# Optimization experiments

Measured on AMD Instinct MI355X. Metric: run time of the kernel, lower is better.

Reference implementation:

```python
import jax, jax.numpy as jnp
import numpy as np

EPS = 1e-5

def _layer_norm(x, w, b):
    mu = jnp.mean(x, axis=-1, keepdims=True)
    var = jnp.mean(jnp.square(x - mu), axis=-1, keepdims=True)
    return (x - mu) * jax.lax.rsqrt(var + EPS) * w + b

def setup_inputs() -> dict:
    B, N, C, H, CH = 1, 256, 128, 4, 32
    key = jax.random.key(0)
    ks = jax.random.split(key, 8)
    s = 0.02
    return {
        "z": jax.random.normal(ks[0], (B, N, N, C), dtype=jnp.float32),
        "pair_mask": jnp.ones((B, N, N), dtype=jnp.float32),
        "ln_w": jnp.ones((C,), dtype=jnp.float32),
        "ln_b": jnp.zeros((C,), dtype=jnp.float32),
        "Wq": jax.random.normal(ks[1], (H * CH, C), dtype=jnp.float32) * s,
        "Wk": jax.random.normal(ks[2], (H * CH, C), dtype=jnp.float32) * s,
        "Wv": jax.random.normal(ks[3], (H * CH, C), dtype=jnp.float32) * s,
        "Wb": jax.random.normal(ks[4], (H, C), dtype=jnp.float32) * s,
        "Wg": jax.random.normal(ks[5], (H * CH, C), dtype=jnp.float32) * s,
        "bg": jnp.zeros((H * CH,), dtype=jnp.float32),
        "Wo": jax.random.normal(ks[6], (C, H * CH), dtype=jnp.float32) * s,
        "bo": jnp.zeros((C,), dtype=jnp.float32),
    }

def reference(z, pair_mask, ln_w, ln_b, Wq, Wk, Wv, Wb, Wg, bg, Wo, bo):
    B, I, J, C = z.shape
    H = Wb.shape[0]
    CH = Wq.shape[0] // H
    zn = _layer_norm(z, ln_w, ln_b)                      # (B,I,J,C)
    q = (zn @ Wq.T).reshape(B, I, J, H, CH)
    k = (zn @ Wk.T).reshape(B, I, J, H, CH)
    v = (zn @ Wv.T).reshape(B, I, J, H, CH)
    bias = zn @ Wb.T                                     # (B,I,J,H) -> per-head pair bias
    g = jax.nn.sigmoid(zn @ Wg.T + bg)                   # (B,I,J,H*CH)
    scale = 1.0 / jnp.sqrt(jnp.asarray(CH, z.dtype))
    # logits[b,h,i,j,k] = q_ij . k_ik / sqrt(CH) + bias[b,h,j,k]
    logits = jnp.einsum('bijhd,bikhd->bhijk', q, k) * scale
    logits = logits + jnp.transpose(bias, (0, 3, 1, 2))[:, :, None, :, :]
    # pair mask: (B,i,j,k) outer product, True = attend
    mask2d = (pair_mask[..., :, None] * pair_mask[..., None, :]) > 0.5
    logits = jnp.where(mask2d[:, None], logits, jnp.asarray(-1e9, logits.dtype))
    probs = jax.nn.softmax(logits, axis=-1)
    o = jnp.einsum('bhijk,bikhd->bijhd', probs, v).reshape(B, I, J, H * CH)
    o = g * o
    return o @ Wo.T + bo
```

## Files before the change

### kernel.cpp

```cpp
#include <hip/hip_runtime.h>
#include <hip/hip_bf16.h>

#define ATT_SCALE 0.17677669529663687f
#define LOG2E     1.4426950408889634f

typedef __attribute__((ext_vector_type(8))) short short8v;
typedef __attribute__((ext_vector_type(4))) float f32x4;
typedef __attribute__((ext_vector_type(16))) float f32x16;

__device__ __forceinline__ short f2bf(float f) {
    unsigned u = __builtin_bit_cast(unsigned, f);
    u = u + 0x7fffu + ((u >> 16) & 1u);
    return (short)(u >> 16);
}
__device__ __forceinline__ float bf2f(short s) {
    unsigned u = ((unsigned)(unsigned short)s) << 16;
    return __builtin_bit_cast(float, u);
}
__device__ __forceinline__ unsigned pk2(float lo, float hi) {
    return (unsigned)(unsigned short)f2bf(lo) |
           ((unsigned)(unsigned short)f2bf(hi) << 16);
}
__device__ __forceinline__ float lo16f(unsigned w) {
    return __builtin_bit_cast(float, w << 16);
}
__device__ __forceinline__ float hi16f(unsigned w) {
    return __builtin_bit_cast(float, w & 0xffff0000u);
}
__device__ __forceinline__ float exp2i(float x) {
    float r;
    asm("v_exp_f32 %0, %1" : "=v"(r) : "v"(x));
    return r;
}
__device__ __forceinline__ unsigned short f2h(float f) {
    _Float16 h = (_Float16)f;
    return __builtin_bit_cast(unsigned short, h);
}
__device__ __forceinline__ float h2f(unsigned short u) {
    return (float)__builtin_bit_cast(_Float16, u);
}

__global__ __launch_bounds__(256) void k_wprep(
    const float* __restrict__ Wq, const float* __restrict__ Wk,
    const float* __restrict__ Wv, const float* __restrict__ Wg,
    const float* __restrict__ Wb, const float* __restrict__ Wo,
    unsigned short* __restrict__ wbf, unsigned short* __restrict__ wbbf,
    unsigned short* __restrict__ wohi, unsigned short* __restrict__ wolo)
{
    int idx = blockIdx.x * 256 + threadIdx.x;
    if (idx < 65536) {
        int m = idx >> 14, e = idx & 16383;
        float v;
        if (m == 0)      v = Wq[e] * (ATT_SCALE * LOG2E);
        else if (m == 1) v = Wk[e];
        else if (m == 2) v = Wv[e];
        else             v = Wg[e];
        wbf[idx] = (unsigned short)f2bf(v);
    } else if (idx < 66048) {
        int e = idx - 65536;
        wbbf[e] = (unsigned short)f2bf(Wb[e]);
    } else if (idx < 82432) {
        int e = idx - 66048;
        float w = Wo[e];
        short hv = f2bf(w);
        wohi[e] = (unsigned short)hv;
        wolo[e] = (unsigned short)f2bf(w - bf2f(hv));
    }
}

__global__ __launch_bounds__(512, 4) void k_lnproj(
    const float* __restrict__ z, const float* __restrict__ lnw,
    const float* __restrict__ lnb,
    const unsigned short* __restrict__ wbf, const unsigned short* __restrict__ wbbf,
    const float* __restrict__ bg,
    unsigned short* __restrict__ q_o, unsigned short* __restrict__ k_o,
    unsigned short* __restrict__ vt_o, unsigned short* __restrict__ g_o,
    unsigned short* __restrict__ bbf)
{
    __shared__ __align__(16) short zn[128][136];
    __shared__ __align__(16) short wstg[8][32][40];

    const int tid  = threadIdx.x;
    const int lane = tid & 63;
    const int wave = tid >> 6;
    const int l15  = lane & 15;
    const int g    = lane >> 4;
    const int wr   = wave >> 2;
    const int wc   = wave & 3;
    const long p0  = (long)blockIdx.x * 128;
    const int xq   = (int)(p0 >> 8);
    const int y0   = (int)(p0 & 255);

    {
        const int r = tid >> 2, q4 = tid & 3;
        const float* zrow = z + (p0 + r) * 128 + q4 * 32;
        float4 xv[8];
        float s1 = 0.f, s2 = 0.f;
#pragma unroll
        for (int m = 0; m < 8; ++m) {
            xv[m] = *(const float4*)(zrow + m * 4);
            s1 += xv[m].x + xv[m].y + xv[m].z + xv[m].w;
            s2 += xv[m].x * xv[m].x + xv[m].y * xv[m].y +
                  xv[m].z * xv[m].z + xv[m].w * xv[m].w;
        }
        s1 += __shfl_xor(s1, 1); s2 += __shfl_xor(s2, 1);
        s1 += __shfl_xor(s1, 2); s2 += __shfl_xor(s2, 2);
        float mu  = s1 * 0.0078125f;
        float inv = rsqrtf(s2 * 0.0078125f - mu * mu + 1e-5f);
#pragma unroll
        for (int mm = 0; mm < 4; ++mm) {
            float4 a = xv[2 * mm], b = xv[2 * mm + 1];
            const float* wp = lnw + q4 * 32 + mm * 8;
            const float* bp = lnb + q4 * 32 + mm * 8;
            float4 w0 = *(const float4*)wp, w1 = *(const float4*)(wp + 4);
            float4 b0 = *(const float4*)bp, b1 = *(const float4*)(bp + 4);
            uint4 uu;
            uu.x = pk2((a.x - mu) * inv * w0.x + b0.x, (a.y - mu) * inv * w0.y + b0.y);
            uu.y = pk2((a.z - mu) * inv * w0.z + b0.z, (a.w - mu) * inv * w0.w + b0.w);
            uu.z = pk2((b.x - mu) * inv * w1.x + b1.x, (b.y - mu) * inv * w1.y + b1.y);
            uu.w = pk2((b.z - mu) * inv * w1.z + b1.z, (b.w - mu) * inv * w1.w + b1.w);
            *(uint4*)&zn[r][q4 * 32 + mm * 8] = uu;
        }
    }
    __syncthreads();

    if (wc == 0) {
        const unsigned short* wbp = wbbf + (l15 & 3) * 128;
        short8v wb[4];
#pragma unroll
        for (int ks = 0; ks < 4; ++ks)
            wb[ks] = *(const short8v*)(wbp + ks * 32 + g * 8);
        f32x4 bacc[4];
#pragma unroll
        for (int rt = 0; rt < 4; ++rt) bacc[rt] = (f32x4){0.f, 0.f, 0.f, 0.f};
#pragma unroll
        for (int ks = 0; ks < 4; ++ks)
#pragma unroll
            for (int rt = 0; rt < 4; ++rt) {
                short8v a = *(const short8v*)&zn[wr * 64 + rt * 16 + l15][ks * 32 + g * 8];
                bacc[rt] = __builtin_amdgcn_mfma_f32_16x16x32_bf16(a, wb[ks], bacc[rt], 0, 0, 0);
            }
        if (l15 < 4) {
#pragma unroll
            for (int rt = 0; rt < 4; ++rt) {
                uint2 w;
                w.x = pk2(bacc[rt][0] * LOG2E, bacc[rt][1] * LOG2E);
                w.y = pk2(bacc[rt][2] * LOG2E, bacc[rt][3] * LOG2E);
                *(uint2*)(bbf + (long)l15 * 65536 + xq * 256 + y0 +
                          wr * 64 + rt * 16 + g * 4) = w;
            }
        }
    }

    for (int wsel = 0; wsel < 4; ++wsel) {
        const unsigned short* __restrict__ W = wbf + wsel * 16384;
        f32x4 acc[4][2];
#pragma unroll
        for (int rt = 0; rt < 4; ++rt) {
            acc[rt][0] = (f32x4){0.f, 0.f, 0.f, 0.f};
            acc[rt][1] = (f32x4){0.f, 0.f, 0.f, 0.f};
        }
#pragma unroll
        for (int ks = 0; ks < 4; ++ks) {
            short8v b0 = *(const short8v*)(W + (wc * 32 + l15) * 128 + ks * 32 + g * 8);
            short8v b1 = *(const short8v*)(W + (wc * 32 + 16 + l15) * 128 + ks * 32 + g * 8);
#pragma unroll
            for (int rt = 0; rt < 4; ++rt) {
                short8v a = *(const short8v*)&zn[wr * 64 + rt * 16 + l15][ks * 32 + g * 8];
                acc[rt][0] = __builtin_amdgcn_mfma_f32_16x16x32_bf16(a, b0, acc[rt][0], 0, 0, 0);
                acc[rt][1] = __builtin_amdgcn_mfma_f32_16x16x32_bf16(a, b1, acc[rt][1], 0, 0, 0);
            }
        }

        if (wsel == 3) {
#pragma unroll
            for (int ct = 0; ct < 2; ++ct) {
                float bgc = bg[wc * 32 + ct * 16 + l15];
#pragma unroll
                for (int rt = 0; rt < 4; ++rt)
#pragma unroll
                    for (int r = 0; r < 4; ++r) {
                        float val = acc[rt][ct][r] + bgc;
                        g_o[((long)wc * 65536 + p0 + wr * 64 + rt * 16 + g * 4 + r) * 32 +
                            ct * 16 + l15] = f2h(1.0f / (1.0f + __expf(-val)));
                    }
            }
        } else if (wsel == 2) {
#pragma unroll
            for (int pair = 0; pair < 2; ++pair) {
#pragma unroll
                for (int rt2 = 0; rt2 < 2; ++rt2)
#pragma unroll
                    for (int ct = 0; ct < 2; ++ct)
#pragma unroll
                        for (int r = 0; r < 4; ++r)
                            wstg[wave][ct * 16 + l15][rt2 * 16 + g * 4 + r] =
                                f2bf(acc[pair * 2 + rt2][ct][r]);
#pragma unroll
                for (int e = 0; e < 4; ++e) {
                    int idx = e * 64 + lane;
                    int d = idx >> 3, k4 = idx & 7;
                    int k4p = ((k4 & 1) << 1) | ((k4 >> 1) & 1) | (k4 & 4);
                    short4 sv = *(const short4*)&wstg[wave][d][k4 * 4];
                    *(short4*)(vt_o + (((long)wc * 256 + xq) * 32 + d) * 256 +
                               y0 + wr * 64 + pair * 32 + k4p * 4) = sv;
                }
            }
        } else {
            unsigned short* __restrict__ O = (wsel == 0) ? q_o : k_o;
#pragma unroll
            for (int pair = 0; pair < 2; ++pair) {
#pragma unroll
                for (int rt2 = 0; rt2 < 2; ++rt2)
#pragma unroll
                    for (int ct = 0; ct < 2; ++ct)
#pragma unroll
                        for (int r = 0; r < 4; ++r)
                            wstg[wave][rt2 * 16 + g * 4 + r][ct * 16 + l15] =
                                f2bf(acc[pair * 2 + rt2][ct][r]);
#pragma unroll
                for (int ps = 0; ps < 2; ++ps) {
                    int idx = ps * 64 + lane;
                    int lr = idx >> 2, ch = (idx & 3) * 8;
                    short8v vv = *(const short8v*)&wstg[wave][lr][ch];
                    *(short8v*)(O + ((long)wc * 65536 + p0 + wr * 64 + pair * 32 + lr) * 32 + ch) = vv;
                }
            }
        }
    }
}

__global__ __launch_bounds__(256, 2) void k_attn_mfma(
    const unsigned short* __restrict__ q_ws, const unsigned short* __restrict__ k_ws,
    const unsigned short* __restrict__ vt_ws, const unsigned short* __restrict__ g_ws,
    const unsigned short* __restrict__ bbf, const float* __restrict__ pm,
    unsigned short* __restrict__ ob)
{
    __shared__ __align__(16) short Ksh[256][40];
    __shared__ __align__(16) short VTsh[32][264];
    __shared__ float pmsh[256];

    const int tid  = threadIdx.x;
    const int lane = tid & 63;
    const int wave = tid >> 6;
    const int l31  = lane & 31;
    const int hi   = lane >> 5;
    const int h = blockIdx.x & 3;
    const int i = blockIdx.x >> 2;
    const long hbase  = ((long)h * 65536 + (long)i * 256) * 32;
    const long vtbase = ((long)h * 256 + i) * 8192;

    pmsh[tid] = pm[i * 256 + tid];
#pragma unroll
    for (int pass = 0; pass < 4; ++pass) {
        int idx = pass * 256 + tid;
        *(short8v*)&Ksh[idx >> 2][(idx & 3) * 8] =
            *(const short8v*)(k_ws + hbase + idx * 8);
        *(short8v*)&VTsh[idx >> 5][(idx & 31) * 8] =
            *(const short8v*)(vt_ws + vtbase + idx * 8);
    }
    __syncthreads();

    bool ok4 = true;
#pragma unroll
    for (int e = 0; e < 4; ++e) ok4 = ok4 && (pmsh[lane * 4 + e] > 0.5f);
    const bool allok = __all(ok4);

    const f32x16 zero16 = {0.f,0.f,0.f,0.f,0.f,0.f,0.f,0.f,
                           0.f,0.f,0.f,0.f,0.f,0.f,0.f,0.f};

    for (int qi = 0; qi < 2; ++qi) {
        const int qb = wave * 2 + qi;
        const int ql = qb * 32 + l31;

        short8v bq0 = *(const short8v*)(q_ws + hbase + (long)ql * 32 + hi * 8);
        short8v bq1 = *(const short8v*)(q_ws + hbase + (long)ql * 32 + 16 + hi * 8);
        const bool rowok = pmsh[ql] > 0.5f;
        const unsigned short* bp_base = bbf + ((long)h << 16) + (long)ql * 256 + hi * 4;

        f32x16 oacc = zero16;
        float ls0 = 0.f, ls1 = 0.f;

#pragma unroll
        for (int t = 0; t < 8; ++t) {
            uint2 bw0 = *(const uint2*)(bp_base + t * 32);
            uint2 bw1 = *(const uint2*)(bp_base + t * 32 + 8);
            uint2 bw2 = *(const uint2*)(bp_base + t * 32 + 16);
            uint2 bw3 = *(const uint2*)(bp_base + t * 32 + 24);

            short8v ka0 = *(const short8v*)&Ksh[t * 32 + l31][hi * 8];
            short8v ka1 = *(const short8v*)&Ksh[t * 32 + l31][16 + hi * 8];
            __builtin_amdgcn_s_setprio(1);
            f32x16 s = __builtin_amdgcn_mfma_f32_32x32x16_bf16(ka0, bq0, zero16, 0, 0, 0);
            s = __builtin_amdgcn_mfma_f32_32x32x16_bf16(ka1, bq1, s, 0, 0, 0);
            __builtin_amdgcn_s_setprio(0);

            uint4 w0, w1;
            if (allok) {
                float p0, p1, p2, p3;
                p0 = exp2i(s[0] + lo16f(bw0.x)); p1 = exp2i(s[1] + hi16f(bw0.x));
                p2 = exp2i(s[2] + lo16f(bw0.y)); p3 = exp2i(s[3] + hi16f(bw0.y));
                ls0 += (p0 + p1) + (p2 + p3);
                w0.x = pk2(p0, p1); w0.y = pk2(p2, p3);
                p0 = exp2i(s[4] + lo16f(bw1.x)); p1 = exp2i(s[5] + hi16f(bw1.x));
                p2 = exp2i(s[6] + lo16f(bw1.y)); p3 = exp2i(s[7] + hi16f(bw1.y));
                ls1 += (p0 + p1) + (p2 + p3);
                w0.z = pk2(p0, p1); w0.w = pk2(p2, p3);
                p0 = exp2i(s[8] + lo16f(bw2.x)); p1 = exp2i(s[9] + hi16f(bw2.x));
                p2 = exp2i(s[10] + lo16f(bw2.y)); p3 = exp2i(s[11] + hi16f(bw2.y));
                ls0 += (p0 + p1) + (p2 + p3);
                w1.x = pk2(p0, p1); w1.y = pk2(p2, p3);
                p0 = exp2i(s[12] + lo16f(bw3.x)); p1 = exp2i(s[13] + hi16f(bw3.x));
                p2 = exp2i(s[14] + lo16f(bw3.y)); p3 = exp2i(s[15] + hi16f(bw3.y));
                ls1 += (p0 + p1) + (p2 + p3);
                w1.z = pk2(p0, p1); w1.w = pk2(p2, p3);
            } else {
#pragma unroll
                for (int n = 0; n < 4; ++n) {
                    uint2 bw = (n == 0) ? bw0 : (n == 1) ? bw1 : (n == 2) ? bw2 : bw3;
                    f32x4 ma = *(const f32x4*)&pmsh[t * 32 + n * 8 + hi * 4];
                    float p0 = exp2i(rowok ? s[4*n+0] + lo16f(bw.x) + ((ma[0] > 0.5f) ? 0.f : -1e9f) : 0.0f);
                    float p1 = exp2i(rowok ? s[4*n+1] + hi16f(bw.x) + ((ma[1] > 0.5f) ? 0.f : -1e9f) : 0.0f);
                    float p2 = exp2i(rowok ? s[4*n+2] + lo16f(bw.y) + ((ma[2] > 0.5f) ? 0.f : -1e9f) : 0.0f);
                    float p3 = exp2i(rowok ? s[4*n+3] + hi16f(bw.y) + ((ma[3] > 0.5f) ? 0.f : -1e9f) : 0.0f);
                    ls0 += (p0 + p1) + (p2 + p3);
                    unsigned wa = pk2(p0, p1), wb = pk2(p2, p3);
                    if (n == 0) { w0.x = wa; w0.y = wb; }
                    else if (n == 1) { w0.z = wa; w0.w = wb; }
                    else if (n == 2) { w1.x = wa; w1.y = wb; }
                    else { w1.z = wa; w1.w = wb; }
                }
            }
            short8v pb0 = *(short8v*)&w0;
            short8v pb1 = *(short8v*)&w1;

            short8v va0 = *(const short8v*)&VTsh[l31][t * 32 + hi * 8];
            short8v va1 = *(const short8v*)&VTsh[l31][t * 32 + 16 + hi * 8];
            __builtin_amdgcn_s_setprio(1);
            oacc = __builtin_amdgcn_mfma_f32_32x32x16_bf16(va0, pb0, oacc, 0, 0, 0);
            oacc = __builtin_amdgcn_mfma_f32_32x32x16_bf16(va1, pb1, oacc, 0, 0, 0);
            __builtin_amdgcn_s_setprio(0);
        }

        float lsum = ls0 + ls1;
        lsum += __shfl_xor(lsum, 32);
        const float linv = 1.0f / lsum;

        const long grow = hbase + (long)ql * 32;
        const long orow = (long)(i * 256 + ql) * 128 + h * 32;
#pragma unroll
        for (int n = 0; n < 4; ++n) {
            int dbase = n * 8 + hi * 4;
            ushort4 gu = *(const ushort4*)(g_ws + grow + dbase);
            float v0 = oacc[4 * n + 0] * linv * h2f(gu.x);
            float v1 = oacc[4 * n + 1] * linv * h2f(gu.y);
            float v2 = oacc[4 * n + 2] * linv * h2f(gu.z);
            float v3 = oacc[4 * n + 3] * linv * h2f(gu.w);
            short4 sh = {f2bf(v0), f2bf(v1), f2bf(v2), f2bf(v3)};
            *(short4*)(ob + orow + dbase) = sh;
        }
    }
}

__global__ __launch_bounds__(512, 4) void k_outproj(
    const unsigned short* __restrict__ ob,
    const unsigned short* __restrict__ wohi, const unsigned short* __restrict__ wolo,
    const float* __restrict__ bo, float* __restrict__ out)
{
    const int tid  = threadIdx.x;
    const int lane = tid & 63;
    const int wave = tid >> 6;
    const int l15  = lane & 15;
    const int g    = lane >> 4;
    const int wr   = wave >> 2;
    const int wc   = wave & 3;
    const long p0  = (long)blockIdx.x * 128;

    f32x4 acc[4][2];
#pragma unroll
    for (int rt = 0; rt < 4; ++rt) {
        acc[rt][0] = (f32x4){0.f, 0.f, 0.f, 0.f};
        acc[rt][1] = (f32x4){0.f, 0.f, 0.f, 0.f};
    }

#pragma unroll
    for (int ks = 0; ks < 4; ++ks) {
        const int wof = ks * 32 + g * 8;
        short8v bh0 = *(const short8v*)(wohi + (wc * 32 + l15) * 128 + wof);
        short8v bh1 = *(const short8v*)(wohi + (wc * 32 + 16 + l15) * 128 + wof);
        short8v bl0 = *(const short8v*)(wolo + (wc * 32 + l15) * 128 + wof);
        short8v bl1 = *(const short8v*)(wolo + (wc * 32 + 16 + l15) * 128 + wof);
#pragma unroll
        for (int rt = 0; rt < 4; ++rt) {
            long aoff = (p0 + wr * 64 + rt * 16 + l15) * 128 + ks * 32 + g * 8;
            short8v ah = *(const short8v*)(ob + aoff);
            acc[rt][0] = __builtin_amdgcn_mfma_f32_16x16x32_bf16(ah, bh0, acc[rt][0], 0, 0, 0);
            acc[rt][0] = __builtin_amdgcn_mfma_f32_16x16x32_bf16(ah, bl0, acc[rt][0], 0, 0, 0);
            acc[rt][1] = __builtin_amdgcn_mfma_f32_16x16x32_bf16(ah, bh1, acc[rt][1], 0, 0, 0);
            acc[rt][1] = __builtin_amdgcn_mfma_f32_16x16x32_bf16(ah, bl1, acc[rt][1], 0, 0, 0);
        }
    }

#pragma unroll
    for (int ct = 0; ct < 2; ++ct) {
        float bv = bo[wc * 32 + ct * 16 + l15];
#pragma unroll
        for (int rt = 0; rt < 4; ++rt)
#pragma unroll
            for (int r = 0; r < 4; ++r)
                out[(p0 + wr * 64 + rt * 16 + g * 4 + r) * 128 +
                    wc * 32 + ct * 16 + l15] = acc[rt][ct][r] + bv;
    }
}

extern "C" void kernel_launch(void* const* d_in, const int* in_sizes, int n_in,
                              void* d_out, int out_size, void* d_ws, size_t ws_size,
                              hipStream_t stream) {
    const float* z   = (const float*)d_in[0];
    const float* pm  = (const float*)d_in[1];
    const float* lnw = (const float*)d_in[2];
    const float* lnb = (const float*)d_in[3];
    const float* Wq  = (const float*)d_in[4];
    const float* Wk  = (const float*)d_in[5];
    const float* Wv  = (const float*)d_in[6];
    const float* Wb  = (const float*)d_in[7];
    const float* Wg  = (const float*)d_in[8];
    const float* bg  = (const float*)d_in[9];
    const float* Wo  = (const float*)d_in[10];
    const float* bo  = (const float*)d_in[11];
    float* out = (float*)d_out;

    unsigned short* wsS  = (unsigned short*)d_ws;
    unsigned short* wbf  = wsS;
    unsigned short* wbbf = wsS + 65536;
    unsigned short* wohi = wsS + 66048;
    unsigned short* wolo = wsS + 82432;
    unsigned short* bbf  = wsS + 98816;
    unsigned short* qb   = wsS + 360960;
    unsigned short* kb   = qb + 8388608;
    unsigned short* vtb  = kb + 8388608;
    unsigned short* obw  = vtb + 8388608;
    unsigned short* ghw  = obw + 8388608;

    k_wprep<<<322, 256, 0, stream>>>(Wq, Wk, Wv, Wg, Wb, Wo, wbf, wbbf, wohi, wolo);
    k_lnproj<<<512, 512, 0, stream>>>(z, lnw, lnb, wbf, wbbf, bg, qb, kb, vtb, ghw, bbf);
    k_attn_mfma<<<1024, 256, 0, stream>>>(qb, kb, vtb, ghw, bbf, pm, obw);
    k_outproj<<<512, 512, 0, stream>>>(obw, wohi, wolo, bo, out);
}
```

Measured before the change: 104.1 us.

## Transpose pair-bias layout and software-pipeline K/V/bias loads in attention loop

The pair bias is now stored as packed bf16 pairs in a transposed [h][k/2][j] layout, so that for a given k pair, adjacent query rows read consecutive words and the bias loads in the attention kernel coalesce across lanes. The attention inner loop prefetches the next tile's K, V^T fragments and bias words into registers before doing the current tile's MFMAs, and the gate values are loaded up front. This hides LDS and global latency at the cost of more registers, which could lower occupancy. The bias writes in the projection kernel become scattered 4-byte stores.

```diff
diff --git a/kernel.cpp b/kernel.cpp
--- a/kernel.cpp
+++ b/kernel.cpp
@@ -75,7 +75,7 @@
     const float* __restrict__ bg,
     unsigned short* __restrict__ q_o, unsigned short* __restrict__ k_o,
     unsigned short* __restrict__ vt_o, unsigned short* __restrict__ g_o,
-    unsigned short* __restrict__ bbf)
+    unsigned* __restrict__ bTP)
 {
     __shared__ __align__(16) short zn[128][136];
     __shared__ __align__(16) short wstg[8][32][40];
@@ -143,11 +143,11 @@
         if (l15 < 4) {
 #pragma unroll
             for (int rt = 0; rt < 4; ++rt) {
-                uint2 w;
-                w.x = pk2(bacc[rt][0] * LOG2E, bacc[rt][1] * LOG2E);
-                w.y = pk2(bacc[rt][2] * LOG2E, bacc[rt][3] * LOG2E);
-                *(uint2*)(bbf + (long)l15 * 65536 + xq * 256 + y0 +
-                          wr * 64 + rt * 16 + g * 4) = w;
+                int kb = y0 + wr * 64 + rt * 16 + g * 4;
+                unsigned w0 = pk2(bacc[rt][0] * LOG2E, bacc[rt][1] * LOG2E);
+                unsigned w1 = pk2(bacc[rt][2] * LOG2E, bacc[rt][3] * LOG2E);
+                bTP[l15 * 32768 + (kb >> 1) * 256 + xq]       = w0;
+                bTP[l15 * 32768 + ((kb >> 1) + 1) * 256 + xq] = w1;
             }
         }
     }
@@ -233,7 +233,7 @@
 __global__ __launch_bounds__(256, 2) void k_attn_mfma(
     const unsigned short* __restrict__ q_ws, const unsigned short* __restrict__ k_ws,
     const unsigned short* __restrict__ vt_ws, const unsigned short* __restrict__ g_ws,
-    const unsigned short* __restrict__ bbf, const float* __restrict__ pm,
+    const unsigned* __restrict__ bTP, const float* __restrict__ pm,
     unsigned short* __restrict__ ob)
 {
     __shared__ __align__(16) short Ksh[256][40];
@@ -276,20 +276,46 @@
         short8v bq0 = *(const short8v*)(q_ws + hbase + (long)ql * 32 + hi * 8);
         short8v bq1 = *(const short8v*)(q_ws + hbase + (long)ql * 32 + 16 + hi * 8);
         const bool rowok = pmsh[ql] > 0.5f;
-        const unsigned short* bp_base = bbf + ((long)h << 16) + (long)ql * 256 + hi * 4;
+        const unsigned* btp = bTP + h * 32768 + ql;
+
+        const long grow = hbase + (long)ql * 32;
+        ushort4 gu[4];
+#pragma unroll
+        for (int n = 0; n < 4; ++n)
+            gu[n] = *(const ushort4*)(g_ws + grow + n * 8 + hi * 4);
 
         f32x16 oacc = zero16;
         float ls0 = 0.f, ls1 = 0.f;
 
+        short8v ka0 = *(const short8v*)&Ksh[l31][hi * 8];
+        short8v ka1 = *(const short8v*)&Ksh[l31][16 + hi * 8];
+        short8v va0 = *(const short8v*)&VTsh[l31][hi * 8];
+        short8v va1 = *(const short8v*)&VTsh[l31][16 + hi * 8];
+        unsigned bb[8];
+#pragma unroll
+        for (int n = 0; n < 4; ++n) {
+            int m = (n * 8 + hi * 4) >> 1;
+            bb[2 * n]     = btp[m * 256];
+            bb[2 * n + 1] = btp[(m + 1) * 256];
+        }
+
 #pragma unroll
         for (int t = 0; t < 8; ++t) {
-            uint2 bw0 = *(const uint2*)(bp_base + t * 32);
-            uint2 bw1 = *(const uint2*)(bp_base + t * 32 + 8);
-            uint2 bw2 = *(const uint2*)(bp_base + t * 32 + 16);
-            uint2 bw3 = *(const uint2*)(bp_base + t * 32 + 24);
-
-            short8v ka0 = *(const short8v*)&Ksh[t * 32 + l31][hi * 8];
-            short8v ka1 = *(const short8v*)&Ksh[t * 32 + l31][16 + hi * 8];
+            short8v nka0, nka1, nva0, nva1;
+            unsigned nbb[8];
+            if (t < 7) {
+                nka0 = *(const short8v*)&Ksh[(t + 1) * 32 + l31][hi * 8];
+                nka1 = *(const short8v*)&Ksh[(t + 1) * 32 + l31][16 + hi * 8];
+                nva0 = *(const short8v*)&VTsh[l31][(t + 1) * 32 + hi * 8];
+                nva1 = *(const short8v*)&VTsh[l31][(t + 1) * 32 + 16 + hi * 8];
+#pragma unroll
+                for (int n = 0; n < 4; ++n) {
+                    int m = ((t + 1) * 32 + n * 8 + hi * 4) >> 1;
+                    nbb[2 * n]     = btp[m * 256];
+                    nbb[2 * n + 1] = btp[(m + 1) * 256];
+                }
+            }
+
             __builtin_amdgcn_s_setprio(1);
             f32x16 s = __builtin_amdgcn_mfma_f32_32x32x16_bf16(ka0, bq0, zero16, 0, 0, 0);
             s = __builtin_amdgcn_mfma_f32_32x32x16_bf16(ka1, bq1, s, 0, 0, 0);
@@ -298,31 +324,30 @@
             uint4 w0, w1;
             if (allok) {
                 float p0, p1, p2, p3;
-                p0 = exp2i(s[0] + lo16f(bw0.x)); p1 = exp2i(s[1] + hi16f(bw0.x));
-                p2 = exp2i(s[2] + lo16f(bw0.y)); p3 = exp2i(s[3] + hi16f(bw0.y));
+                p0 = exp2i(s[0] + lo16f(bb[0])); p1 = exp2i(s[1] + hi16f(bb[0]));
+                p2 = exp2i(s[2] + lo16f(bb[1])); p3 = exp2i(s[3] + hi16f(bb[1]));
                 ls0 += (p0 + p1) + (p2 + p3);
                 w0.x = pk2(p0, p1); w0.y = pk2(p2, p3);
-                p0 = exp2i(s[4] + lo16f(bw1.x)); p1 = exp2i(s[5] + hi16f(bw1.x));
-                p2 = exp2i(s[6] + lo16f(bw1.y)); p3 = exp2i(s[7] + hi16f(bw1.y));
+                p0 = exp2i(s[4] + lo16f(bb[2])); p1 = exp2i(s[5] + hi16f(bb[2]));
+                p2 = exp2i(s[6] + lo16f(bb[3])); p3 = exp2i(s[7] + hi16f(bb[3]));
                 ls1 += (p0 + p1) + (p2 + p3);
                 w0.z = pk2(p0, p1); w0.w = pk2(p2, p3);
-                p0 = exp2i(s[8] + lo16f(bw2.x)); p1 = exp2i(s[9] + hi16f(bw2.x));
-                p2 = exp2i(s[10] + lo16f(bw2.y)); p3 = exp2i(s[11] + hi16f(bw2.y));
+                p0 = exp2i(s[8] + lo16f(bb[4])); p1 = exp2i(s[9] + hi16f(bb[4]));
+                p2 = exp2i(s[10] + lo16f(bb[5])); p3 = exp2i(s[11] + hi16f(bb[5]));
                 ls0 += (p0 + p1) + (p2 + p3);
                 w1.x = pk2(p0, p1); w1.y = pk2(p2, p3);
-                p0 = exp2i(s[12] + lo16f(bw3.x)); p1 = exp2i(s[13] + hi16f(bw3.x));
-                p2 = exp2i(s[14] + lo16f(bw3.y)); p3 = exp2i(s[15] + hi16f(bw3.y));
+                p0 = exp2i(s[12] + lo16f(bb[6])); p1 = exp2i(s[13] + hi16f(bb[6]));
+                p2 = exp2i(s[14] + lo16f(bb[7])); p3 = exp2i(s[15] + hi16f(bb[7]));
                 ls1 += (p0 + p1) + (p2 + p3);
                 w1.z = pk2(p0, p1); w1.w = pk2(p2, p3);
             } else {
 #pragma unroll
                 for (int n = 0; n < 4; ++n) {
-                    uint2 bw = (n == 0) ? bw0 : (n == 1) ? bw1 : (n == 2) ? bw2 : bw3;
                     f32x4 ma = *(const f32x4*)&pmsh[t * 32 + n * 8 + hi * 4];
-                    float p0 = exp2i(rowok ? s[4*n+0] + lo16f(bw.x) + ((ma[0] > 0.5f) ? 0.f : -1e9f) : 0.0f);
-                    float p1 = exp2i(rowok ? s[4*n+1] + hi16f(bw.x) + ((ma[1] > 0.5f) ? 0.f : -1e9f) : 0.0f);
-                    float p2 = exp2i(rowok ? s[4*n+2] + lo16f(bw.y) + ((ma[2] > 0.5f) ? 0.f : -1e9f) : 0.0f);
-                    float p3 = exp2i(rowok ? s[4*n+3] + hi16f(bw.y) + ((ma[3] > 0.5f) ? 0.f : -1e9f) : 0.0f);
+                    float p0 = exp2i(rowok ? s[4*n+0] + lo16f(bb[2*n])   + ((ma[0] > 0.5f) ? 0.f : -1e9f) : 0.0f);
+                    float p1 = exp2i(rowok ? s[4*n+1] + hi16f(bb[2*n])   + ((ma[1] > 0.5f) ? 0.f : -1e9f) : 0.0f);
+                    float p2 = exp2i(rowok ? s[4*n+2] + lo16f(bb[2*n+1]) + ((ma[2] > 0.5f) ? 0.f : -1e9f) : 0.0f);
+                    float p3 = exp2i(rowok ? s[4*n+3] + hi16f(bb[2*n+1]) + ((ma[3] > 0.5f) ? 0.f : -1e9f) : 0.0f);
                     ls0 += (p0 + p1) + (p2 + p3);
                     unsigned wa = pk2(p0, p1), wb = pk2(p2, p3);
                     if (n == 0) { w0.x = wa; w0.y = wb; }
@@ -334,28 +359,30 @@
             short8v pb0 = *(short8v*)&w0;
             short8v pb1 = *(short8v*)&w1;
 
-            short8v va0 = *(const short8v*)&VTsh[l31][t * 32 + hi * 8];
-            short8v va1 = *(const short8v*)&VTsh[l31][t * 32 + 16 + hi * 8];
             __builtin_amdgcn_s_setprio(1);
             oacc = __builtin_amdgcn_mfma_f32_32x32x16_bf16(va0, pb0, oacc, 0, 0, 0);
             oacc = __builtin_amdgcn_mfma_f32_32x32x16_bf16(va1, pb1, oacc, 0, 0, 0);
             __builtin_amdgcn_s_setprio(0);
+
+            if (t < 7) {
+                ka0 = nka0; ka1 = nka1; va0 = nva0; va1 = nva1;
+#pragma unroll
+                for (int e = 0; e < 8; ++e) bb[e] = nbb[e];
+            }
         }
 
         float lsum = ls0 + ls1;
         lsum += __shfl_xor(lsum, 32);
         const float linv = 1.0f / lsum;
 
-        const long grow = hbase + (long)ql * 32;
         const long orow = (long)(i * 256 + ql) * 128 + h * 32;
 #pragma unroll
         for (int n = 0; n < 4; ++n) {
             int dbase = n * 8 + hi * 4;
-            ushort4 gu = *(const ushort4*)(g_ws + grow + dbase);
-            float v0 = oacc[4 * n + 0] * linv * h2f(gu.x);
-            float v1 = oacc[4 * n + 1] * linv * h2f(gu.y);
-            float v2 = oacc[4 * n + 2] * linv * h2f(gu.z);
-            float v3 = oacc[4 * n + 3] * linv * h2f(gu.w);
+            float v0 = oacc[4 * n + 0] * linv * h2f(gu[n].x);
+            float v1 = oacc[4 * n + 1] * linv * h2f(gu[n].y);
+            float v2 = oacc[4 * n + 2] * linv * h2f(gu[n].z);
+            float v3 = oacc[4 * n + 3] * linv * h2f(gu[n].w);
             short4 sh = {f2bf(v0), f2bf(v1), f2bf(v2), f2bf(v3)};
             *(short4*)(ob + orow + dbase) = sh;
         }
@@ -435,7 +462,7 @@
     unsigned short* wbbf = wsS + 65536;
     unsigned short* wohi = wsS + 66048;
     unsigned short* wolo = wsS + 82432;
-    unsigned short* bbf  = wsS + 98816;
+    unsigned* bTP        = (unsigned*)(wsS + 98816);
     unsigned short* qb   = wsS + 360960;
     unsigned short* kb   = qb + 8388608;
     unsigned short* vtb  = kb + 8388608;
@@ -443,7 +470,7 @@
     unsigned short* ghw  = obw + 8388608;
 
     k_wprep<<<322, 256, 0, stream>>>(Wq, Wk, Wv, Wg, Wb, Wo, wbf, wbbf, wohi, wolo);
-    k_lnproj<<<512, 512, 0, stream>>>(z, lnw, lnb, wbf, wbbf, bg, qb, kb, vtb, ghw, bbf);
-    k_attn_mfma<<<1024, 256, 0, stream>>>(qb, kb, vtb, ghw, bbf, pm, obw);
+    k_lnproj<<<512, 512, 0, stream>>>(z, lnw, lnb, wbf, wbbf, bg, qb, kb, vtb, ghw, bTP);
+    k_attn_mfma<<<1024, 256, 0, stream>>>(qb, kb, vtb, ghw, bTP, pm, obw);
     k_outproj<<<512, 512, 0, stream>>>(obw, wohi, wolo, bo, out);
 }
```

Result: faster. 91.48 us (-12.2%).
